# Performance work log

Hardware: AMD Instinct MI355X
Metric: run time of the kernel (lower is better)

## Reference

```python
import jax, jax.numpy as jnp
import numpy as np

N = 50000      # nodes
E = 800000     # edges (avg degree 16)
H = 256        # h_size
MAXCTX = 8     # max_context


def setup_inputs() -> dict:
    key = jax.random.key(0)
    ks = jax.random.split(key, 6)
    x = jax.random.normal(ks[0], (N, H), jnp.float32)
    edge_index = jax.random.randint(ks[1], (2, E), 0, N)
    node_label = jax.random.randint(ks[2], (N, MAXCTX), 0, N)
    context_len = jax.random.randint(ks[3], (N,), 0, MAXCTX)
    gcn_W = jax.random.normal(ks[4], (H, H), jnp.float32) / np.sqrt(H)
    gcn_b = jnp.zeros((H,), jnp.float32)
    resize_W = jax.random.normal(ks[5], (H * MAXCTX, H), jnp.float32) / np.sqrt(H * MAXCTX)
    resize_b = jnp.zeros((H,), jnp.float32)
    return {"x": x, "edge_index": edge_index, "node_label": node_label,
            "context_len": context_len, "gcn_W": gcn_W, "gcn_b": gcn_b,
            "resize_W": resize_W, "resize_b": resize_b}


def gcn_conv(x, edge_index, W, b, n):
    # PyG GCNConv: add self-loops, symmetric deg^-1/2 normalization, then linear.
    loop = jnp.arange(n)
    src = jnp.concatenate([edge_index[0], loop])
    dst = jnp.concatenate([edge_index[1], loop])
    deg = jax.ops.segment_sum(jnp.ones_like(dst, x.dtype), dst, num_segments=n)
    inv_sqrt = jax.lax.rsqrt(jnp.maximum(deg, 1.0))  # deg>=1 due to self-loops
    h = x @ W                                        # [n, H]
    coef = inv_sqrt[src] * inv_sqrt[dst]             # [E+n]
    out = jax.ops.segment_sum(h[src] * coef[:, None], dst, num_segments=n)
    return out + b


def reference(x, edge_index, node_label, context_len, gcn_W, gcn_b, resize_W, resize_b):
    n = x.shape[0]
    # gcn_layers=2: relu(GCN(x)) (dropout is identity in eval) then GCN again.
    feat = jax.nn.relu(gcn_conv(x, edge_index, gcn_W, gcn_b, n))
    feat = gcn_conv(feat, edge_index, gcn_W, gcn_b, n)
    # Batched variable-length context gather with zero padding.
    ctx = feat[node_label]                                            # [n, MAXCTX, H]
    mask = (jnp.arange(node_label.shape[1])[None, :] < context_len[:, None])
    ctx = ctx * mask[:, :, None].astype(feat.dtype)
    ctx = ctx.reshape(n, -1) @ resize_W + resize_b                    # [n, H]
    return feat * ctx                                                 # rep_vec per node
```

## Files before the change

kernel.cpp:

```cpp
#include <hip/hip_runtime.h>

typedef _Float16 f16;
typedef _Float16 f16x8 __attribute__((ext_vector_type(8)));
typedef float f32x16 __attribute__((ext_vector_type(16)));

#define MFMA(a, b, c) __builtin_amdgcn_mfma_f32_32x32x16_f16(a, b, c, 0, 0, 0)

__device__ __forceinline__ void gload_lds16(const f16* g, f16* l) {
    __builtin_amdgcn_global_load_lds(
        (const __attribute__((address_space(1))) unsigned int*)g,
        (__attribute__((address_space(3))) unsigned int*)l, 16, 0, 0);
}


#define NBMAX 256
#define CHUNK 8192
#define CAP   8192

__global__ __launch_bounds__(256) void bin_count(
        const int* __restrict__ dst, const int* __restrict__ clen,
        int* __restrict__ gbc, int* __restrict__ ghist, int E, int n, int chn) {
    __shared__ int bc[NBMAX];
    __shared__ int ch[9];
    int tid = threadIdx.x;
    bc[tid] = 0;
    if (tid < 9) ch[tid] = 0;
    __syncthreads();
    int e0 = blockIdx.x * CHUNK, e1 = min(e0 + CHUNK, E);
    for (int i = e0 + tid; i < e1; i += 256)
        atomicAdd(&bc[dst[i] >> 8], 1);
    int n0 = blockIdx.x * chn, n1 = min(n0 + chn, n);
    for (int i = n0 + tid; i < n1; i += 256) {
        int l = clen[i]; l = max(0, min(8, l));
        atomicAdd(&ch[l], 1);
    }
    __syncthreads();
    if (bc[tid]) atomicAdd(&gbc[tid], bc[tid]);
    if (tid < 9 && ch[tid]) atomicAdd(&ghist[tid], ch[tid]);
}

__global__ __launch_bounds__(256) void scan_small(
        const int* __restrict__ gbc, int* __restrict__ gbase,
        const int* __restrict__ ghist, int* __restrict__ chbase, int nb, int E) {
    __shared__ int s[NBMAX];
    int tid = threadIdx.x;
    int v = (tid < nb) ? gbc[tid] : 0;
    s[tid] = v;
    __syncthreads();
    for (int off = 1; off < 256; off <<= 1) {
        int u = (tid >= off) ? s[tid - off] : 0;
        __syncthreads();
        s[tid] += u;
        __syncthreads();
    }
    if (tid <= nb) gbase[tid] = (tid < nb) ? s[tid] - v : E;
    if (tid == 0) {
        int run = 0;
        for (int i = 0; i < 9; ++i) { int c = ghist[i]; chbase[i] = run; run += c; }
    }
}

__global__ __launch_bounds__(256) void bin_scatter(
        const int* __restrict__ src, const int* __restrict__ dst,
        const int* __restrict__ clen,
        const int* __restrict__ gbase, int* __restrict__ gfill,
        const int* __restrict__ chbase, int* __restrict__ chfill,
        int2* __restrict__ binned, int* __restrict__ perm, int* __restrict__ plen,
        int E, int n, int chn) {
    __shared__ int bc[NBMAX], bb[NBMAX];
    __shared__ int cc[9], cb[9];
    int tid = threadIdx.x;
    bc[tid] = 0;
    if (tid < 9) cc[tid] = 0;
    __syncthreads();
    int e0 = blockIdx.x * CHUNK, e1 = min(e0 + CHUNK, E);
    for (int i = e0 + tid; i < e1; i += 256)
        atomicAdd(&bc[dst[i] >> 8], 1);
    int n0 = blockIdx.x * chn, n1 = min(n0 + chn, n);
    for (int i = n0 + tid; i < n1; i += 256) {
        int l = clen[i]; l = max(0, min(8, l));
        atomicAdd(&cc[l], 1);
    }
    __syncthreads();
    {
        int c = bc[tid];
        bb[tid] = c ? gbase[tid] + atomicAdd(&gfill[tid], c) : 0;
        bc[tid] = 0;
    }
    if (tid < 9) {
        int c = cc[tid];
        cb[tid] = c ? chbase[tid] + atomicAdd(&chfill[tid], c) : 0;
        cc[tid] = 0;
    }
    __syncthreads();
    for (int i = e0 + tid; i < e1; i += 256) {
        int d = dst[i], b = d >> 8;
        int p = bb[b] + atomicAdd(&bc[b], 1);
        binned[p] = make_int2(src[i], d);
    }
    for (int i = n0 + tid; i < n1; i += 256) {
        int l = clen[i]; l = max(0, min(8, l));
        int p = cb[l] + atomicAdd(&cc[l], 1);
        perm[p] = i;
        plen[p] = l;
    }
}

__global__ __launch_bounds__(256) void csr_build(
        const int2* __restrict__ binned, const int* __restrict__ gbase,
        int* __restrict__ row_ptr, float* __restrict__ inv_s,
        int* __restrict__ ew, int E, int n) {
    __shared__ int cnt[256], base[256], fill[256];
    __shared__ int ebuf[CAP];
    int tid = threadIdx.x, b = blockIdx.x;
    int e0 = gbase[b], e1 = gbase[b + 1], sz = e1 - e0;
    cnt[tid] = 0;
    __syncthreads();
    for (int i = e0 + tid; i < e1; i += 256)
        atomicAdd(&cnt[binned[i].y & 255], 1);
    __syncthreads();
    int v = cnt[tid];
    base[tid] = v;
    __syncthreads();
    for (int off = 1; off < 256; off <<= 1) {
        int u = (tid >= off) ? base[tid - off] : 0;
        __syncthreads();
        base[tid] += u;
        __syncthreads();
    }
    int ex = base[tid] - v;
    base[tid] = ex;
    fill[tid] = 0;
    int node = b * 256 + tid;
    if (node < n) {
        row_ptr[node] = e0 + ex;
        inv_s[node] = rsqrtf((float)(v + 1));
    }
    if (b == 0 && tid == 0) row_ptr[n] = E;
    __syncthreads();
    for (int i = e0 + tid; i < e1; i += 256) {
        int2 q = binned[i];
        int lo = q.y & 255;
        int p = base[lo] + atomicAdd(&fill[lo], 1);
        if (p < CAP) ebuf[p] = q.x; else ew[e0 + p] = q.x;
    }
    __syncthreads();
    int lim = min(sz, CAP);
    for (int p = tid; p < lim; p += 256) ew[e0 + p] = ebuf[p];
}

__global__ __launch_bounds__(256) void pre_trans(
        const float* __restrict__ gW, f16* __restrict__ Wth, f16* __restrict__ Wtl,
        const float* __restrict__ rW, f16* __restrict__ Rth, f16* __restrict__ Rtl) {
    int b = blockIdx.x;
    __shared__ f16 Th[64][68], Tl[64][68];
    const float* src; f16 *dh, *dl; int K, k0, n0;
    if (b < 128) { src = rW; dh = Rth; dl = Rtl; K = 2048; k0 = (b >> 2) * 64; n0 = (b & 3) * 64; }
    else { int bb = b - 128; src = gW; dh = Wth; dl = Wtl; K = 256; k0 = (bb >> 2) * 64; n0 = (bb & 3) * 64; }
    int c = threadIdx.x & 63, r0 = threadIdx.x >> 6;
    for (int rr = r0; rr < 64; rr += 4) {
        float v = src[(size_t)(k0 + rr) * 256 + n0 + c];
        f16 h = (f16)v;
        Th[rr][c] = h; Tl[rr][c] = (f16)(v - (float)h);
    }
    __syncthreads();
    int k = threadIdx.x & 63, nr0 = threadIdx.x >> 6;
    for (int nn = nr0; nn < 64; nn += 4) {
        size_t oidx = (size_t)(n0 + nn) * K + k0 + k;
        dh[oidx] = Th[k][nn];
        dl[oidx] = Tl[k][nn];
    }
}


union H4 { f16 f[4]; ushort4 u; };

__global__ __launch_bounds__(512, 4) void agg_split(const float* __restrict__ X,
        const int* __restrict__ ew, const int* __restrict__ rp,
        const float* __restrict__ invs, f16* __restrict__ ohi, f16* __restrict__ olo, int n) {
    __shared__ float part[4][256];
    int w = threadIdx.x >> 6, lane = threadIdx.x & 63;
    int local = w >> 1, half = w & 1;
    int node = blockIdx.x * 4 + local;
    bool active = node < n;
    float4 acc = make_float4(0.f, 0.f, 0.f, 0.f);
    float si = 0.f;
    if (active) {
        si = invs[node];
        int e0 = rp[node], e1 = rp[node + 1];
        int mid = e0 + ((e1 - e0 + 1) >> 1);
        int lo = half ? mid : e0;
        int hi = half ? e1 : mid;
        if (!half) {
            float4 a = *((const float4*)(X + (size_t)node * 256) + lane);
            acc = make_float4(a.x * si, a.y * si, a.z * si, a.w * si);
        }
        int e = lo;
        for (; e + 8 <= hi; e += 8) {
            int q[8]; float ws[8]; float4 v[8];
            #pragma unroll
            for (int u = 0; u < 8; ++u) q[u] = ew[e + u];
            #pragma unroll
            for (int u = 0; u < 8; ++u) ws[u] = invs[q[u]];
            #pragma unroll
            for (int u = 0; u < 8; ++u) v[u] = *((const float4*)(X + (size_t)q[u] * 256) + lane);
            #pragma unroll
            for (int u = 0; u < 8; ++u) {
                acc.x = fmaf(ws[u], v[u].x, acc.x); acc.y = fmaf(ws[u], v[u].y, acc.y);
                acc.z = fmaf(ws[u], v[u].z, acc.z); acc.w = fmaf(ws[u], v[u].w, acc.w);
            }
        }
        for (; e < hi; ++e) {
            int q = ew[e];
            float wq = invs[q];
            float4 v = *((const float4*)(X + (size_t)q * 256) + lane);
            acc.x = fmaf(wq, v.x, acc.x); acc.y = fmaf(wq, v.y, acc.y);
            acc.z = fmaf(wq, v.z, acc.z); acc.w = fmaf(wq, v.w, acc.w);
        }
    }
    if (half) *(float4*)&part[local][lane * 4] = acc;
    __syncthreads();
    if (!half && active) {
        float4 o = *(const float4*)&part[local][lane * 4];
        float v0 = si * (acc.x + o.x), v1 = si * (acc.y + o.y);
        float v2 = si * (acc.z + o.z), v3 = si * (acc.w + o.w);
        H4 hh, ll;
        f16 h;
        h = (f16)v0; hh.f[0] = h; ll.f[0] = (f16)(v0 - (float)h);
        h = (f16)v1; hh.f[1] = h; ll.f[1] = (f16)(v1 - (float)h);
        h = (f16)v2; hh.f[2] = h; ll.f[2] = (f16)(v2 - (float)h);
        h = (f16)v3; hh.f[3] = h; ll.f[3] = (f16)(v3 - (float)h);
        size_t off = (size_t)node * 256 + lane * 4;
        *(ushort4*)(ohi + off) = hh.u;
        *(ushort4*)(olo + off) = ll.u;
    }
}


__global__ __launch_bounds__(256, 4) void gemm_reg(
        const f16* __restrict__ Ahi, const f16* __restrict__ Alo,
        const f16* __restrict__ Wth, const f16* __restrict__ Wtl,
        const float* __restrict__ bias,
        float* __restrict__ Of32, f16* __restrict__ Ohi, f16* __restrict__ Olo,
        int M, int relu) {
    int tid = threadIdx.x, w = tid >> 6, lane = tid & 63;
    int row0 = blockIdx.x * 32;
    int m = lane & 31, kh = lane >> 5;

    int ar = row0 + m; if (ar >= M) ar = M - 1;
    const f16* pAh = Ahi + (size_t)ar * 256 + kh * 8;
    const f16* pAl = Alo + (size_t)ar * 256 + kh * 8;
    const f16* pBh[2]; const f16* pBl[2];
    #pragma unroll
    for (int t = 0; t < 2; ++t) {
        int nn = w * 64 + t * 32 + m;
        pBh[t] = Wth + (size_t)nn * 256 + kh * 8;
        pBl[t] = Wtl + (size_t)nn * 256 + kh * 8;
    }

    f32x16 acc[2] = {};
    #pragma unroll 4
    for (int k8 = 0; k8 < 16; ++k8) {
        f16x8 ah = *(const f16x8*)(pAh + k8 * 16);
        f16x8 al = *(const f16x8*)(pAl + k8 * 16);
        #pragma unroll
        for (int t = 0; t < 2; ++t) {
            f16x8 bh = *(const f16x8*)(pBh[t] + k8 * 16);
            f16x8 bl = *(const f16x8*)(pBl[t] + k8 * 16);
            acc[t] = MFMA(ah, bh, acc[t]);
            acc[t] = MFMA(ah, bl, acc[t]);
            acc[t] = MFMA(al, bh, acc[t]);
        }
    }

    #pragma unroll
    for (int t = 0; t < 2; ++t) {
        int col = w * 64 + t * 32 + m;
        float bv = bias[col];
        #pragma unroll
        for (int r = 0; r < 16; ++r) {
            int row = row0 + (r & 3) + 8 * (r >> 2) + 4 * kh;
            if (row < M) {
                float v = acc[t][r] + bv;
                if (relu) v = fmaxf(v, 0.f);
                size_t idx = (size_t)row * 256 + col;
                if (Of32) Of32[idx] = v;
                if (Ohi) {
                    f16 h = (f16)v;
                    Ohi[idx] = h; Olo[idx] = (f16)(v - (float)h);
                }
            }
        }
    }
}


__global__ __launch_bounds__(256, 3) void ctx_gemm(
        const f16* __restrict__ fhi, const f16* __restrict__ flo,
        const int* __restrict__ perm, const int* __restrict__ plen,
        const int* __restrict__ label,
        const f16* __restrict__ Rth, const f16* __restrict__ Rtl,
        const float* __restrict__ rbias, float* __restrict__ out,
        const f16* __restrict__ zp, int M) {
    __shared__ __align__(16) f16 LA[3][2][4096];
    __shared__ int s_lbl[8][64];
    __shared__ int s_perm[64];
    __shared__ int s_max;
    int tid = threadIdx.x, w = tid >> 6, lane = tid & 63;
    int row0 = (int)(gridDim.x - 1 - blockIdx.x) * 64;
    int m = lane & 31, kh = lane >> 5;

    if (tid == 0) s_max = 0;
    __syncthreads();
    if (tid < 64) {
        int r = row0 + tid;
        int p = (r < M) ? perm[r] : -1;
        s_perm[tid] = p;
        int len = (r < M) ? plen[r] : 0;
        atomicMax(&s_max, len);
        int4 l0 = make_int4(-1, -1, -1, -1), l1 = l0;
        if (p >= 0) {
            l0 = *(const int4*)(label + (size_t)p * 8);
            l1 = *(const int4*)(label + (size_t)p * 8 + 4);
        }
        s_lbl[0][tid] = (0 < len) ? l0.x : -1;
        s_lbl[1][tid] = (1 < len) ? l0.y : -1;
        s_lbl[2][tid] = (2 < len) ? l0.z : -1;
        s_lbl[3][tid] = (3 < len) ? l0.w : -1;
        s_lbl[4][tid] = (4 < len) ? l1.x : -1;
        s_lbl[5][tid] = (5 < len) ? l1.y : -1;
        s_lbl[6][tid] = (6 < len) ? l1.z : -1;
        s_lbl[7][tid] = (7 < len) ? l1.w : -1;
    }
    __syncthreads();
    int T = s_max * 4;

    f32x16 acc[2][2] = {};

    if (T > 0) {
        #define STAGE(t_, b_)                                                     \
        {                                                                         \
            int j_ = (t_) >> 2, k0e_ = ((t_) & 3) * 64;                           \
            int rl_ = lane >> 3;                                                  \
            int k8s_ = (lane & 7) ^ rl_;                                          \
            _Pragma("unroll")                                                     \
            for (int q = 0; q < 4; ++q) {                                         \
                int o_ = w * 4 + q;                                               \
                int mat_ = o_ >> 3, rg_ = o_ & 7;                                 \
                int lbl_ = s_lbl[j_][rg_ * 8 + rl_];                              \
                const f16* base_ = mat_ ? flo : fhi;                              \
                const f16* g_ = (lbl_ >= 0)                                       \
                    ? base_ + (size_t)lbl_ * 256 + k0e_ + k8s_ * 8 : zp;          \
                gload_lds16(g_, &LA[b_][mat_][rg_ * 512]);                        \
            }                                                                     \
        }
        STAGE(0, 0);
        if (T > 1) STAGE(1, 1);
        asm volatile("s_waitcnt vmcnt(0)" ::: "memory");
        __builtin_amdgcn_s_barrier();
        __builtin_amdgcn_sched_barrier(0);
        for (int t = 0; t < T; ++t) {
            int b = t % 3;
            int j = t >> 2, k0e = (t & 3) * 64;
            f16x8 Bh[4][2], Bl[4][2];
            #pragma unroll
            for (int jt = 0; jt < 2; ++jt) {
                int nn = w * 64 + jt * 32 + m;
                size_t boff = (size_t)nn * 2048 + j * 256 + k0e + kh * 8;
                const f16* ph = Rth + boff;
                const f16* pl = Rtl + boff;
                #pragma unroll
                for (int s = 0; s < 4; ++s) {
                    Bh[s][jt] = *(const f16x8*)(ph + s * 16);
                    Bl[s][jt] = *(const f16x8*)(pl + s * 16);
                }
            }
            __builtin_amdgcn_sched_barrier(0);
            if (t + 2 < T) STAGE(t + 2, (t + 2) % 3);
            __builtin_amdgcn_sched_barrier(0);
            #pragma unroll
            for (int s = 0; s < 4; ++s) {
                int k8 = s * 2 + kh;
                int slot = (k8 ^ (m & 7)) * 8;
                f16x8 ah[2], al[2];
                #pragma unroll
                for (int i = 0; i < 2; ++i) {
                    int ro = (i * 32 + m) * 64;
                    ah[i] = *(const f16x8*)&LA[b][0][ro + slot];
                    al[i] = *(const f16x8*)&LA[b][1][ro + slot];
                }
                #pragma unroll
                for (int jt = 0; jt < 2; ++jt) {
                    #pragma unroll
                    for (int i = 0; i < 2; ++i) {
                        acc[i][jt] = MFMA(ah[i], Bh[s][jt], acc[i][jt]);
                        acc[i][jt] = MFMA(ah[i], Bl[s][jt], acc[i][jt]);
                        acc[i][jt] = MFMA(al[i], Bh[s][jt], acc[i][jt]);
                    }
                }
            }
            if (t + 2 < T) {
                asm volatile("s_waitcnt vmcnt(4)" ::: "memory");
            } else {
                asm volatile("s_waitcnt vmcnt(0)" ::: "memory");
            }
            __builtin_amdgcn_s_barrier();
            __builtin_amdgcn_sched_barrier(0);
        }
        #undef STAGE
    }

    #pragma unroll
    for (int jt = 0; jt < 2; ++jt) {
        int col = w * 64 + jt * 32 + m;
        float rbv = rbias[col];
        #pragma unroll
        for (int i = 0; i < 2; ++i) {
            #pragma unroll
            for (int r = 0; r < 16; ++r) {
                int lr = i * 32 + (r & 3) + 8 * (r >> 2) + 4 * kh;
                int p = s_perm[lr];
                if (p >= 0) {
                    size_t idx = (size_t)p * 256 + col;
                    float f2 = (float)fhi[idx] + (float)flo[idx];
                    out[idx] = f2 * (acc[i][jt][r] + rbv);
                }
            }
        }
    }
}


extern "C" void kernel_launch(void* const* d_in, const int* in_sizes, int n_in,
                              void* d_out, int out_size, void* d_ws, size_t ws_size,
                              hipStream_t stream) {
    const float* x    = (const float*)d_in[0];
    const int*   edge = (const int*)d_in[1];
    const int*   lbl  = (const int*)d_in[2];
    const int*   clen = (const int*)d_in[3];
    const float* gW   = (const float*)d_in[4];
    const float* gb   = (const float*)d_in[5];
    const float* rW   = (const float*)d_in[6];
    const float* rb   = (const float*)d_in[7];

    const int N = in_sizes[3];
    const int E = in_sizes[1] / 2;

    char* ws = (char*)d_ws;
    size_t off = 0;
    auto take = [&](size_t bytes) -> char* {
        char* p = ws + off;
        off = (off + bytes + 255) & ~(size_t)255;
        return p;
    };
    int*   g_small  = (int*)take(1024 * sizeof(int));
    int*   g_bcnt   = g_small;
    int*   g_bbase  = g_small + 256;
    int*   g_bfill  = g_small + 520;
    int*   g_chist  = g_small + 776;
    int*   g_chbase = g_small + 792;
    int*   g_chfill = g_small + 808;
    int*   row_ptr = (int*)take((size_t)(N + 1) * sizeof(int));
    int*   ew      = (int*)take((size_t)E * sizeof(int));
    int*   perm    = (int*)take((size_t)N * sizeof(int));
    int*   plen    = (int*)take((size_t)N * sizeof(int));
    float* inv_s   = (float*)take((size_t)N * sizeof(float));
    f16*   zp      = (f16*)take(1024);
    f16*   Wth     = (f16*)take((size_t)256 * 256 * sizeof(f16));
    f16*   Wtl     = (f16*)take((size_t)256 * 256 * sizeof(f16));
    f16*   Rth     = (f16*)take((size_t)256 * 2048 * sizeof(f16));
    f16*   Rtl     = (f16*)take((size_t)256 * 2048 * sizeof(f16));
    f16*   Ahi     = (f16*)take((size_t)N * 256 * sizeof(f16));
    f16*   Alo     = (f16*)take((size_t)N * 256 * sizeof(f16));
    float* Y1      = (float*)take((size_t)N * 256 * sizeof(float));
    f16*   Fhi     = (f16*)take((size_t)N * 256 * sizeof(f16));
    f16*   Flo     = (f16*)take((size_t)N * 256 * sizeof(f16));
    int2*  binned  = (int2*)Y1;

    hipMemsetAsync(g_small, 0, 1024 * sizeof(int), stream);
    hipMemsetAsync(zp, 0, 1024, stream);

    int NB   = (N + 255) >> 8;
    int GBIN = (E + CHUNK - 1) / CHUNK;
    int CHN  = (N + GBIN - 1) / GBIN;

    bin_count<<<GBIN, 256, 0, stream>>>(edge + E, clen, g_bcnt, g_chist, E, N, CHN);
    scan_small<<<1, 256, 0, stream>>>(g_bcnt, g_bbase, g_chist, g_chbase, NB, E);
    bin_scatter<<<GBIN, 256, 0, stream>>>(edge, edge + E, clen, g_bbase, g_bfill,
                                          g_chbase, g_chfill, binned, perm, plen,
                                          E, N, CHN);
    csr_build<<<NB, 256, 0, stream>>>(binned, g_bbase, row_ptr, inv_s, ew, E, N);
    pre_trans<<<144, 256, 0, stream>>>(gW, Wth, Wtl, rW, Rth, Rtl);

    int gB32 = (N + 31) / 32;
    int gB64 = (N + 63) / 64;
    agg_split<<<(N + 3) / 4, 512, 0, stream>>>(x, ew, row_ptr, inv_s, Ahi, Alo, N);
    gemm_reg<<<gB32, 256, 0, stream>>>(Ahi, Alo, Wth, Wtl, gb, Y1, nullptr, nullptr, N, 1);
    agg_split<<<(N + 3) / 4, 512, 0, stream>>>(Y1, ew, row_ptr, inv_s, Ahi, Alo, N);
    gemm_reg<<<gB32, 256, 0, stream>>>(Ahi, Alo, Wth, Wtl, gb, nullptr, Fhi, Flo, N, 0);
    ctx_gemm<<<gB64, 256, 0, stream>>>(Fhi, Flo, perm, plen, lbl, Rth, Rtl,
                                       rb, (float*)d_out, zp, N);
}
```

Before: 726.2 us.

## Stage GEMM A-tiles through LDS with triple buffering; fuse weight transpose into bin_count

Replaces the register-only 32-row GEMM with a 64-row-tile GEMM. It streams the hi/lo A operands into a swizzled, triple-buffered LDS pipeline using direct global-to-LDS loads, so each B fragment is reused across two row subtiles. It also folds the weight transpose/split kernel into extra blocks of the bin_count launch, removing one kernel launch. The cost is lower occupancy (launch bounds drop from 4 to 3 blocks per CU), more LDS use, and manual waitcnt/barrier scheduling that must stay correct.

```diff
diff --git a/kernel.cpp b/kernel.cpp
--- a/kernel.cpp
+++ b/kernel.cpp
@@ -17,12 +17,36 @@
 #define CHUNK 8192
 #define CAP   8192
 
-__global__ __launch_bounds__(256) void bin_count(
+__global__ __launch_bounds__(256) void bin_count_trans(
         const int* __restrict__ dst, const int* __restrict__ clen,
-        int* __restrict__ gbc, int* __restrict__ ghist, int E, int n, int chn) {
+        int* __restrict__ gbc, int* __restrict__ ghist, int E, int n, int chn,
+        int nbc,
+        const float* __restrict__ gW, f16* __restrict__ Wth, f16* __restrict__ Wtl,
+        const float* __restrict__ rW, f16* __restrict__ Rth, f16* __restrict__ Rtl) {
     __shared__ int bc[NBMAX];
     __shared__ int ch[9];
+    __shared__ f16 Th[64][68], Tl[64][68];
     int tid = threadIdx.x;
+    if ((int)blockIdx.x >= nbc) {
+        int b = (int)blockIdx.x - nbc;
+        const float* src; f16 *dh, *dl; int K, k0, n0;
+        if (b < 128) { src = rW; dh = Rth; dl = Rtl; K = 2048; k0 = (b >> 2) * 64; n0 = (b & 3) * 64; }
+        else { int bb = b - 128; src = gW; dh = Wth; dl = Wtl; K = 256; k0 = (bb >> 2) * 64; n0 = (bb & 3) * 64; }
+        int c = tid & 63, r0 = tid >> 6;
+        for (int rr = r0; rr < 64; rr += 4) {
+            float v = src[(size_t)(k0 + rr) * 256 + n0 + c];
+            f16 h = (f16)v;
+            Th[rr][c] = h; Tl[rr][c] = (f16)(v - (float)h);
+        }
+        __syncthreads();
+        int k = tid & 63, nr0 = tid >> 6;
+        for (int nn = nr0; nn < 64; nn += 4) {
+            size_t oidx = (size_t)(n0 + nn) * K + k0 + k;
+            dh[oidx] = Th[k][nn];
+            dl[oidx] = Tl[k][nn];
+        }
+        return;
+    }
     bc[tid] = 0;
     if (tid < 9) ch[tid] = 0;
     __syncthreads();
@@ -147,29 +171,6 @@
     __syncthreads();
     int lim = min(sz, CAP);
     for (int p = tid; p < lim; p += 256) ew[e0 + p] = ebuf[p];
-}
-
-__global__ __launch_bounds__(256) void pre_trans(
-        const float* __restrict__ gW, f16* __restrict__ Wth, f16* __restrict__ Wtl,
-        const float* __restrict__ rW, f16* __restrict__ Rth, f16* __restrict__ Rtl) {
-    int b = blockIdx.x;
-    __shared__ f16 Th[64][68], Tl[64][68];
-    const float* src; f16 *dh, *dl; int K, k0, n0;
-    if (b < 128) { src = rW; dh = Rth; dl = Rtl; K = 2048; k0 = (b >> 2) * 64; n0 = (b & 3) * 64; }
-    else { int bb = b - 128; src = gW; dh = Wth; dl = Wtl; K = 256; k0 = (bb >> 2) * 64; n0 = (bb & 3) * 64; }
-    int c = threadIdx.x & 63, r0 = threadIdx.x >> 6;
-    for (int rr = r0; rr < 64; rr += 4) {
-        float v = src[(size_t)(k0 + rr) * 256 + n0 + c];
-        f16 h = (f16)v;
-        Th[rr][c] = h; Tl[rr][c] = (f16)(v - (float)h);
-    }
-    __syncthreads();
-    int k = threadIdx.x & 63, nr0 = threadIdx.x >> 6;
-    for (int nn = nr0; nn < 64; nn += 4) {
-        size_t oidx = (size_t)(n0 + nn) * K + k0 + k;
-        dh[oidx] = Th[k][nn];
-        dl[oidx] = Tl[k][nn];
-    }
 }
 
 
@@ -237,57 +238,111 @@
 }
 
 
-__global__ __launch_bounds__(256, 4) void gemm_reg(
+__global__ __launch_bounds__(256, 3) void gemm_lds(
         const f16* __restrict__ Ahi, const f16* __restrict__ Alo,
         const f16* __restrict__ Wth, const f16* __restrict__ Wtl,
         const float* __restrict__ bias,
         float* __restrict__ Of32, f16* __restrict__ Ohi, f16* __restrict__ Olo,
         int M, int relu) {
+    __shared__ __align__(16) f16 LA[3][2][4096];
     int tid = threadIdx.x, w = tid >> 6, lane = tid & 63;
-    int row0 = blockIdx.x * 32;
+    int row0 = (int)blockIdx.x * 64;
     int m = lane & 31, kh = lane >> 5;
-
-    int ar = row0 + m; if (ar >= M) ar = M - 1;
-    const f16* pAh = Ahi + (size_t)ar * 256 + kh * 8;
-    const f16* pAl = Alo + (size_t)ar * 256 + kh * 8;
-    const f16* pBh[2]; const f16* pBl[2];
+    const int T = 4;
+
+    f32x16 acc[2][2] = {};
+
+    {
+        #define STAGE(t_, b_)                                                     \
+        {                                                                         \
+            int k0e_ = (t_) * 64;                                                 \
+            int rl_ = lane >> 3;                                                  \
+            int k8s_ = (lane & 7) ^ rl_;                                          \
+            _Pragma("unroll")                                                     \
+            for (int q = 0; q < 4; ++q) {                                         \
+                int o_ = w * 4 + q;                                               \
+                int mat_ = o_ >> 3, rg_ = o_ & 7;                                 \
+                int r_ = row0 + rg_ * 8 + rl_;                                    \
+                if (r_ >= M) r_ = M - 1;                                          \
+                const f16* base_ = mat_ ? Alo : Ahi;                              \
+                const f16* g_ = base_ + (size_t)r_ * 256 + k0e_ + k8s_ * 8;       \
+                gload_lds16(g_, &LA[b_][mat_][rg_ * 512]);                        \
+            }                                                                     \
+        }
+        STAGE(0, 0);
+        STAGE(1, 1);
+        asm volatile("s_waitcnt vmcnt(0)" ::: "memory");
+        __builtin_amdgcn_s_barrier();
+        __builtin_amdgcn_sched_barrier(0);
+        for (int t = 0; t < T; ++t) {
+            int b = t % 3;
+            int k0e = t * 64;
+            f16x8 Bh[4][2], Bl[4][2];
+            #pragma unroll
+            for (int jt = 0; jt < 2; ++jt) {
+                int nn = w * 64 + jt * 32 + m;
+                size_t boff = (size_t)nn * 256 + k0e + kh * 8;
+                const f16* ph = Wth + boff;
+                const f16* pl = Wtl + boff;
+                #pragma unroll
+                for (int s = 0; s < 4; ++s) {
+                    Bh[s][jt] = *(const f16x8*)(ph + s * 16);
+                    Bl[s][jt] = *(const f16x8*)(pl + s * 16);
+                }
+            }
+            __builtin_amdgcn_sched_barrier(0);
+            if (t + 2 < T) STAGE(t + 2, (t + 2) % 3);
+            __builtin_amdgcn_sched_barrier(0);
+            #pragma unroll
+            for (int s = 0; s < 4; ++s) {
+                int k8 = s * 2 + kh;
+                int slot = (k8 ^ (m & 7)) * 8;
+                f16x8 ah[2], al[2];
+                #pragma unroll
+                for (int i = 0; i < 2; ++i) {
+                    int ro = (i * 32 + m) * 64;
+                    ah[i] = *(const f16x8*)&LA[b][0][ro + slot];
+                    al[i] = *(const f16x8*)&LA[b][1][ro + slot];
+                }
+                #pragma unroll
+                for (int jt = 0; jt < 2; ++jt) {
+                    #pragma unroll
+                    for (int i = 0; i < 2; ++i) {
+                        acc[i][jt] = MFMA(ah[i], Bh[s][jt], acc[i][jt]);
+                        acc[i][jt] = MFMA(ah[i], Bl[s][jt], acc[i][jt]);
+                        acc[i][jt] = MFMA(al[i], Bh[s][jt], acc[i][jt]);
+                    }
+                }
+            }
+            if (t + 2 < T) {
+                asm volatile("s_waitcnt vmcnt(4)" ::: "memory");
+            } else {
+                asm volatile("s_waitcnt vmcnt(0)" ::: "memory");
+            }
+            __builtin_amdgcn_s_barrier();
+            __builtin_amdgcn_sched_barrier(0);
+        }
+        #undef STAGE
+    }
+
     #pragma unroll
-    for (int t = 0; t < 2; ++t) {
-        int nn = w * 64 + t * 32 + m;
-        pBh[t] = Wth + (size_t)nn * 256 + kh * 8;
-        pBl[t] = Wtl + (size_t)nn * 256 + kh * 8;
-    }
-
-    f32x16 acc[2] = {};
-    #pragma unroll 4
-    for (int k8 = 0; k8 < 16; ++k8) {
-        f16x8 ah = *(const f16x8*)(pAh + k8 * 16);
-        f16x8 al = *(const f16x8*)(pAl + k8 * 16);
-        #pragma unroll
-        for (int t = 0; t < 2; ++t) {
-            f16x8 bh = *(const f16x8*)(pBh[t] + k8 * 16);
-            f16x8 bl = *(const f16x8*)(pBl[t] + k8 * 16);
-            acc[t] = MFMA(ah, bh, acc[t]);
-            acc[t] = MFMA(ah, bl, acc[t]);
-            acc[t] = MFMA(al, bh, acc[t]);
-        }
-    }
-
-    #pragma unroll
-    for (int t = 0; t < 2; ++t) {
-        int col = w * 64 + t * 32 + m;
+    for (int jt = 0; jt < 2; ++jt) {
+        int col = w * 64 + jt * 32 + m;
         float bv = bias[col];
         #pragma unroll
-        for (int r = 0; r < 16; ++r) {
-            int row = row0 + (r & 3) + 8 * (r >> 2) + 4 * kh;
-            if (row < M) {
-                float v = acc[t][r] + bv;
-                if (relu) v = fmaxf(v, 0.f);
-                size_t idx = (size_t)row * 256 + col;
-                if (Of32) Of32[idx] = v;
-                if (Ohi) {
-                    f16 h = (f16)v;
-                    Ohi[idx] = h; Olo[idx] = (f16)(v - (float)h);
+        for (int i = 0; i < 2; ++i) {
+            #pragma unroll
+            for (int r = 0; r < 16; ++r) {
+                int row = row0 + i * 32 + (r & 3) + 8 * (r >> 2) + 4 * kh;
+                if (row < M) {
+                    float v = acc[i][jt][r] + bv;
+                    if (relu) v = fmaxf(v, 0.f);
+                    size_t idx = (size_t)row * 256 + col;
+                    if (Of32) Of32[idx] = v;
+                    if (Ohi) {
+                        f16 h = (f16)v;
+                        Ohi[idx] = h; Olo[idx] = (f16)(v - (float)h);
+                    }
                 }
             }
         }
@@ -484,20 +539,20 @@
     int GBIN = (E + CHUNK - 1) / CHUNK;
     int CHN  = (N + GBIN - 1) / GBIN;
 
-    bin_count<<<GBIN, 256, 0, stream>>>(edge + E, clen, g_bcnt, g_chist, E, N, CHN);
+    bin_count_trans<<<GBIN + 144, 256, 0, stream>>>(edge + E, clen, g_bcnt, g_chist,
+                                                    E, N, CHN, GBIN,
+                                                    gW, Wth, Wtl, rW, Rth, Rtl);
     scan_small<<<1, 256, 0, stream>>>(g_bcnt, g_bbase, g_chist, g_chbase, NB, E);
     bin_scatter<<<GBIN, 256, 0, stream>>>(edge, edge + E, clen, g_bbase, g_bfill,
                                           g_chbase, g_chfill, binned, perm, plen,
                                           E, N, CHN);
     csr_build<<<NB, 256, 0, stream>>>(binned, g_bbase, row_ptr, inv_s, ew, E, N);
-    pre_trans<<<144, 256, 0, stream>>>(gW, Wth, Wtl, rW, Rth, Rtl);
-
-    int gB32 = (N + 31) / 32;
+
     int gB64 = (N + 63) / 64;
     agg_split<<<(N + 3) / 4, 512, 0, stream>>>(x, ew, row_ptr, inv_s, Ahi, Alo, N);
-    gemm_reg<<<gB32, 256, 0, stream>>>(Ahi, Alo, Wth, Wtl, gb, Y1, nullptr, nullptr, N, 1);
+    gemm_lds<<<gB64, 256, 0, stream>>>(Ahi, Alo, Wth, Wtl, gb, Y1, nullptr, nullptr, N, 1);
     agg_split<<<(N + 3) / 4, 512, 0, stream>>>(Y1, ew, row_ptr, inv_s, Ahi, Alo, N);
-    gemm_reg<<<gB32, 256, 0, stream>>>(Ahi, Alo, Wth, Wtl, gb, nullptr, Fhi, Flo, N, 0);
+    gemm_lds<<<gB64, 256, 0, stream>>>(Ahi, Alo, Wth, Wtl, gb, nullptr, Fhi, Flo, N, 0);
     ctx_gemm<<<gB64, 256, 0, stream>>>(Fhi, Flo, perm, plen, lbl, Rth, Rtl,
                                        rb, (float*)d_out, zp, N);
 }
```

Measured after the change: 670.7 us. 1.08x faster.
